# Optimization experiments

Measured on AMD Instinct MI355X. Metric: run time of the kernel, lower is better.

## Reference

```python
import jax, jax.numpy as jnp
import numpy as np

B, N, R, S, H, D, HIDDEN = 4, 1028, 4, 32, 12, 64, 32
L = (2 * S - 1) ** 2  # 3969 relative-position bins


def _build_tables():
    # CPB relative-coordinate table (signed log1p-normalized offsets)
    rng = np.arange(-(S - 1), S, dtype=np.float32)
    dY, dX = np.meshgrid(rng, rng, indexing='ij')
    rel = np.stack([dY / max(S - 1, 1), dX / max(S - 1, 1)], -1).reshape(-1, 2)
    rel_table = np.sign(rel) * np.log1p(np.abs(rel))  # [L, 2]
    # 2D relative-position index table over the SxS patch grid
    Y, X = np.meshgrid(np.arange(S), np.arange(S), indexing='ij')
    flat = np.stack([Y, X], 0).reshape(2, -1)          # [2, P]
    d = flat[:, :, None] - flat[:, None, :]            # [2, P, P]
    d = np.transpose(d, (1, 2, 0)).copy()              # [P, P, 2]
    d[:, :, 0] += S - 1
    d[:, :, 1] += S - 1
    d[:, :, 0] *= 2 * S - 1
    l_idx = d.sum(-1)                                  # [P, P] in [0, L)
    idx = np.full((N, N), -1, dtype=np.int64)          # -1 sentinel for register tokens
    idx[R:, R:] = l_idx
    return jnp.asarray(rel_table, jnp.float32), jnp.asarray(idx)


def setup_inputs() -> dict:
    key = jax.random.key(0)
    ks = jax.random.split(key, 8)
    rel_table, idx_table = _build_tables()
    return {
        'q': jax.random.normal(ks[0], (B, H, N, D), jnp.float32),
        'k': jax.random.normal(ks[1], (B, H, N, D), jnp.float32),
        'v': jax.random.normal(ks[2], (B, H, N, D), jnp.float32),
        'mu': jax.random.normal(ks[3], (B, 2 * H, N), jnp.float32),
        'rel_table': rel_table,                              # [L, 2] buffer
        'W1': jax.random.normal(ks[4], (HIDDEN, 2), jnp.float32) * 0.5,
        'b1': jax.random.normal(ks[5], (HIDDEN,), jnp.float32) * 0.1,
        'W2': jax.random.normal(ks[6], (H, HIDDEN), jnp.float32) * 0.05,
        'gamma': jax.random.normal(ks[7], (H,), jnp.float32),
        'idx_table': idx_table,                              # [N, N] int64
    }


def reference(q, k, v, mu, rel_table, W1, b1, W2, gamma, idx_table):
    # CPB MLP: Linear(2->hidden) + exact GELU + Linear(hidden->H, no bias)
    hid = jax.nn.gelu(rel_table @ W1.T + b1, approximate=False)   # [L, HIDDEN]
    bt = hid @ W2.T                                               # [L, H]
    bt_ext = jnp.concatenate([jnp.zeros((1, H), bt.dtype), bt], 0)  # [L+1, H]
    bias = bt_ext[idx_table + 1]                                  # [N, N, H]; sentinel -1 -> zero row

    # per-token gates: signed log1p transform then q-side + k-side split
    mu_t = jnp.sign(mu) * jnp.log1p(jnp.abs(mu))                  # [B, 2H, N]
    mu_q, mu_k = mu_t[:, :H], mu_t[:, H:]                         # each [B, H, N]
    g = mu_q[:, :, :, None] + mu_k[:, :, None, :]                 # [B, H, N, N]
    gam = jax.nn.sigmoid(gamma)[None, :, None, None]              # [1, H, 1, 1]

    scale = 1.0 / jnp.sqrt(jnp.asarray(D, jnp.float32))
    scores = jnp.einsum('bhqd,bhkd->bhqk', q, k) * scale
    scores = scores + gam * g * jnp.transpose(bias, (2, 0, 1))[None]  # [B, H, N, N]
    attn = jax.nn.softmax(scores, axis=-1)
    return jnp.einsum('bhqk,bhkd->bhqd', attn, v)
```

## Files before the change

kernel.cpp:

```cpp
#include <hip/hip_runtime.h>

#define B_ 4
#define H_ 12
#define N_ 1028
#define D_ 64
#define R_ 4
#define L_ 3969
#define HID_ 32
#define KBLK 64
#define NT_ 17
#define NBH_ (B_*H_)
#define QBLK 256
#define NQT 5
#define NWG (NBH_*NQT)
#define MUTP 1088
#define LOG2E 1.4426950408889634f
#define SCL1 (0.125f*LOG2E)

typedef __attribute__((ext_vector_type(8)))  short bf16x8;
typedef __attribute__((ext_vector_type(2)))  float f32x2;
typedef __attribute__((ext_vector_type(4)))  float f32x4;
typedef __attribute__((ext_vector_type(16))) float f32x16;
typedef __attribute__((ext_vector_type(2)))  unsigned int u32x2;
typedef __attribute__((ext_vector_type(4)))  unsigned int u32x4;

__device__ __forceinline__ unsigned pkbf(float lo, float hi) {
  unsigned r;
  asm("v_cvt_pk_bf16_f32 %0, %1, %2" : "=v"(r) : "v"(lo), "v"(hi));
  return r;
}
__device__ __forceinline__ float exp2_fast(float x) {
  float r; asm("v_exp_f32 %0, %1" : "=v"(r) : "v"(x)); return r;
}
__device__ __forceinline__ float sgnlog1p(float x) {
  float t = log1pf(fabsf(x));
  return (x > 0.f) ? t : ((x < 0.f) ? -t : 0.f);
}

__global__ __launch_bounds__(256) void btmu_kernel(
    const float* __restrict__ rel, const float* __restrict__ W1,
    const float* __restrict__ b1, const float* __restrict__ W2,
    const float* __restrict__ mug, float* __restrict__ bt,
    float* __restrict__ mut) {
  const int blk = blockIdx.x;
  const int tid = threadIdx.x;
  if (blk < 16) {
    int l = blk * 256 + tid;
    if (l >= L_) return;
    float r0 = rel[2*l], r1 = rel[2*l+1];
    float hid[HID_];
#pragma unroll
    for (int j = 0; j < HID_; ++j) {
      float x = W1[2*j]*r0 + W1[2*j+1]*r1 + b1[j];
      hid[j] = 0.5f * x * (1.f + erff(x * 0.70710678118654752f));
    }
#pragma unroll
    for (int h = 0; h < H_; ++h) {
      float acc = 0.f;
#pragma unroll
      for (int j = 0; j < HID_; ++j) acc += W2[h*HID_+j]*hid[j];
      bt[h*L_ + l] = acc;
    }
  } else {
    int idx = (blk - 16) * 256 + tid;
    if (idx >= NBH_*MUTP) return;
    int bh = idx / MUTP, n = idx - bh*MUTP;
    int b = bh / H_, h = bh - b*H_;
    int nc = n < N_ ? n : N_-1;
    mut[bh*MUTP + n] = sgnlog1p(mug[((size_t)b*2*H_ + H_ + h)*N_ + nc]);
  }
}

__global__ __launch_bounds__(512, 2) void attn_kernel(
    const float* __restrict__ qg, const float* __restrict__ kg_,
    const float* __restrict__ vg, const float* __restrict__ mug,
    const float* __restrict__ gammag, const float* __restrict__ btg_g,
    const float* __restrict__ mut, float* __restrict__ outg)
{
  __shared__ __align__(16) float btgs[L_ + 4];
  __shared__ __align__(16) unsigned short Kl[2][64*64];
  __shared__ __align__(16) unsigned short Vl[2][64*64];

  const int tid  = threadIdx.x;
  const int w    = tid >> 6;
  const int lane = tid & 63;
  const int hi   = lane >> 5;
  const int c    = lane & 31;

  const int orig = blockIdx.x;
  const int wg   = (orig & 7) * (NWG/8) + (orig >> 3);
  const int bh   = wg / NQT;
  const int qt   = wg - bh * NQT;
  const int b    = bh / H_;
  const int h    = bh - b * H_;
  const int q0   = qt * QBLK;

  const float gam  = 1.f / (1.f + __expf(-gammag[h]));
  const float gscl = gam * LOG2E;
  for (int i = tid; i < L_; i += 512) btgs[4 + i] = gscl * btg_g[h*L_ + i];
  if (tid < 4) btgs[tid] = 0.f;

  const float* qb = qg  + (size_t)bh*N_*D_;
  const float* kb = kg_ + (size_t)bh*N_*D_;
  const float* vb = vg  + (size_t)bh*N_*D_;
  const float* mt = mut + bh*MUTP;

  const int qrow = q0 + 32*w + c;
  const int qrc  = qrow < N_ ? qrow : N_-1;
  bf16x8 qf[4];
#pragma unroll
  for (int m = 0; m < 4; ++m) {
    const float* p = qb + (size_t)qrc*D_ + 16*m + 8*hi;
    f32x4 a0 = *(const f32x4*)p;
    f32x4 a1 = *(const f32x4*)(p + 4);
    u32x4 qw;
    qw[0] = pkbf(a0[0]*SCL1, a0[1]*SCL1); qw[1] = pkbf(a0[2]*SCL1, a0[3]*SCL1);
    qw[2] = pkbf(a1[0]*SCL1, a1[1]*SCL1); qw[3] = pkbf(a1[2]*SCL1, a1[3]*SCL1);
    qf[m] = __builtin_bit_cast(bf16x8, qw);
  }
  const float muq_c = (qrow < N_) ? sgnlog1p(mug[((size_t)b*2*H_ + h)*N_ + qrow]) : 0.f;
  const int  qi  = qrow - R_;
  const bool qok = (qi >= 0) && (qrow < N_);
  const int  qy  = qi >> 5, qx = qi & 31;
  const int  lqc = qy*63 + qx + 1988;

  const int skr = tid >> 3;
  const int so  = tid & 7;
  const int vkc0 = (tid & 15) * 4;
  const int vdp  = (tid >> 4) * 2;
  const int vkc0p = ((vkc0 >> 1) & 4) | ((vkc0 << 1) & 8) | (vkc0 & 48);

  f32x4 ka0_, ka1_;
  f32x2 vpre[4];
  auto issue = [&](int tt) {
    const int k0n = tt * KBLK;
    {
      int kr = k0n + skr; if (kr >= N_) kr = N_-1;
      const float* p = kb + (size_t)kr*D_ + 8*so;
      ka0_ = *(const f32x4*)p;
      ka1_ = *(const f32x4*)(p + 4);
    }
#pragma unroll
    for (int i = 0; i < 4; ++i) {
      int kr = k0n + vkc0 + i; if (kr >= N_) kr = N_-1;
      vpre[i] = *(const f32x2*)(vb + (size_t)kr*D_ + vdp);
    }
  };

  float mrun = -3.0e38f, lrun = 0.f;
  f32x16 Ot[2];
#pragma unroll
  for (int blk = 0; blk < 2; ++blk)
#pragma unroll
    for (int r = 0; r < 16; ++r) Ot[blk][r] = 0.f;

  issue(0);

  for (int t = 0; t < NT_; ++t) {
    const int k0 = t * KBLK;
    const int p  = t & 1;
    {
      u32x4 kw;
      kw[0] = pkbf(ka0_[0], ka0_[1]); kw[1] = pkbf(ka0_[2], ka0_[3]);
      kw[2] = pkbf(ka1_[0], ka1_[1]); kw[3] = pkbf(ka1_[2], ka1_[3]);
      *(u32x4*)&Kl[p][skr*64 + ((8*so) ^ ((skr & 7) << 3))] = kw;
#pragma unroll
      for (int dd = 0; dd < 2; ++dd) {
        int d = vdp + dd;
        u32x2 vw = (u32x2){pkbf(vpre[0][dd], vpre[1][dd]), pkbf(vpre[2][dd], vpre[3][dd])};
        *(u32x2*)&Vl[p][d*64 + (vkc0p ^ ((d & 7) << 3))] = vw;
      }
    }
    if (t + 1 < NT_) issue(t + 1);
    __syncthreads();

    f32x4 mkv[2][4];
#pragma unroll
    for (int bb = 0; bb < 2; ++bb)
#pragma unroll
      for (int r2 = 0; r2 < 4; ++r2)
        mkv[bb][r2] = *(const f32x4*)&mt[k0 + 32*bb + 8*r2 + 4*hi];

    f32x16 sc[2];
#pragma unroll
    for (int bb = 0; bb < 2; ++bb)
#pragma unroll
      for (int r = 0; r < 16; ++r) sc[bb][r] = 0.f;
    __builtin_amdgcn_s_setprio(1);
#pragma unroll
    for (int m = 0; m < 4; ++m) {
      int sw = (c & 7) << 3;
      bf16x8 ka0 = *(const bf16x8*)&Kl[p][c*64        + ((16*m + 8*hi) ^ sw)];
      bf16x8 ka1 = *(const bf16x8*)&Kl[p][(32+c)*64   + ((16*m + 8*hi) ^ sw)];
      sc[0] = __builtin_amdgcn_mfma_f32_32x32x16_bf16(ka0, qf[m], sc[0], 0, 0, 0);
      sc[1] = __builtin_amdgcn_mfma_f32_32x32x16_bf16(ka1, qf[m], sc[1], 0, 0, 0);
    }
    __builtin_amdgcn_s_setprio(0);

    float smax = -3.0e38f;
#pragma unroll
    for (int bb = 0; bb < 2; ++bb) {
#pragma unroll
      for (int r2 = 0; r2 < 4; ++r2) {
        const f32x4 mk = mkv[bb][r2];
        int base_kc = 32*bb + 8*r2 + 4*hi;
        int ki0 = k0 + base_kc - R_;
        int lk  = (ki0 >> 5)*63 + (ki0 & 31);
        int va  = lqc - lk;
        bool okq = ((unsigned)ki0 < 1024u) && qok;
        int basep = okq ? va : 3;
        f32x4 bv;
        bv[0] = btgs[basep-3]; bv[1] = btgs[basep-2];
        bv[2] = btgs[basep-1]; bv[3] = btgs[basep];
        bool maskq = (ki0 < 1024);
#pragma unroll
        for (int rr = 0; rr < 4; ++rr) {
          float val = sc[bb][4*r2+rr] + (muq_c + mk[rr]) * bv[3-rr];
          val = maskq ? val : -3.0e38f;
          sc[bb][4*r2+rr] = val;
          smax = fmaxf(smax, val);
        }
      }
    }
    smax = fmaxf(smax, __shfl_xor(smax, 32));

    if (__any(smax > mrun)) {
      float mnew = fmaxf(mrun, smax);
      float corr = exp2_fast(mrun - mnew);
      lrun *= corr;
#pragma unroll
      for (int blk = 0; blk < 2; ++blk)
#pragma unroll
        for (int r = 0; r < 16; ++r) Ot[blk][r] *= corr;
      mrun = mnew;
    }

    float psum = 0.f;
#pragma unroll
    for (int bb = 0; bb < 2; ++bb)
#pragma unroll
      for (int r = 0; r < 16; ++r) {
        float pv = exp2_fast(sc[bb][r] - mrun);
        sc[bb][r] = pv;
        psum += pv;
      }
    psum += __shfl_xor(psum, 32);
    lrun += psum;

    u32x4 pa[4];
#pragma unroll
    for (int mm = 0; mm < 4; ++mm) {
      int bb = mm >> 1, s = (mm & 1) * 8;
#pragma unroll
      for (int j = 0; j < 4; ++j)
        pa[mm][j] = pkbf(sc[bb][s + 2*j], sc[bb][s + 2*j + 1]);
    }

    __builtin_amdgcn_s_setprio(1);
#pragma unroll
    for (int mm = 0; mm < 4; ++mm) {
      bf16x8 pfr = __builtin_bit_cast(bf16x8, pa[mm]);
      int sw = (c & 7) << 3;
      bf16x8 va0 = *(const bf16x8*)&Vl[p][c*64      + ((16*mm + 8*hi) ^ sw)];
      bf16x8 va1 = *(const bf16x8*)&Vl[p][(32+c)*64 + ((16*mm + 8*hi) ^ sw)];
      Ot[0] = __builtin_amdgcn_mfma_f32_32x32x16_bf16(va0, pfr, Ot[0], 0, 0, 0);
      Ot[1] = __builtin_amdgcn_mfma_f32_32x32x16_bf16(va1, pfr, Ot[1], 0, 0, 0);
    }
    __builtin_amdgcn_s_setprio(0);
  }

  float rlv = 1.f / lrun;
  const int qo = q0 + 32*w + c;
  if (qo < N_) {
    float* ob = outg + ((size_t)bh*N_ + qo)*D_;
#pragma unroll
    for (int blk = 0; blk < 2; ++blk)
#pragma unroll
      for (int r2 = 0; r2 < 4; ++r2) {
        int dbase = 8*r2 + 4*hi + 32*blk;
        f32x4 ov;
#pragma unroll
        for (int rr = 0; rr < 4; ++rr) ov[rr] = Ot[blk][4*r2+rr] * rlv;
        *(f32x4*)(ob + dbase) = ov;
      }
  }
}

extern "C" void kernel_launch(void* const* d_in, const int* in_sizes, int n_in,
                              void* d_out, int out_size, void* d_ws, size_t ws_size,
                              hipStream_t stream) {
  const float* q     = (const float*)d_in[0];
  const float* k     = (const float*)d_in[1];
  const float* v     = (const float*)d_in[2];
  const float* mu    = (const float*)d_in[3];
  const float* rel   = (const float*)d_in[4];
  const float* W1    = (const float*)d_in[5];
  const float* b1    = (const float*)d_in[6];
  const float* W2    = (const float*)d_in[7];
  const float* gamma = (const float*)d_in[8];

  float* bt  = (float*)d_ws;
  float* mut = bt + H_*L_;

  const int mutblocks = (NBH_*MUTP + 255) / 256;
  btmu_kernel<<<dim3(16 + mutblocks), dim3(256), 0, stream>>>(rel, W1, b1, W2, mu, bt, mut);
  attn_kernel<<<dim3(NWG), dim3(512), 0, stream>>>(q, k, v, mu, gamma, bt, mut,
                                                   (float*)d_out);
}
```

Measured before the change: 61.63 us.

## Split key range across two workgroups with a separate log-sum-exp combine kernel

Each (batch, head, query-tile) attention pass is now split across two workgroups that cover the two halves of the key blocks. Each workgroup writes unnormalized partial outputs plus its running max and sum, and a new combine kernel merges them. Query tiles shrink to 128 rows with 256-thread workgroups, which raises the workgroup count for better CU occupancy. The bias table is stored as bf16 and the gamma scale is folded into the precomputed mu table. The trade-off is an extra kernel launch, partial-output traffic through global memory, and some bf16 rounding of the bias values.

```diff
diff --git a/kernel.cpp b/kernel.cpp
--- a/kernel.cpp
+++ b/kernel.cpp
@@ -9,10 +9,12 @@
 #define HID_ 32
 #define KBLK 64
 #define NT_ 17
-#define NBH_ (B_*H_)
-#define QBLK 256
-#define NQT 5
-#define NWG (NBH_*NQT)
+#define NBH_ 48
+#define QBLK 128
+#define NQT 9
+#define KS_ 2
+#define NWG (NBH_*NQT*KS_)
+#define NROW (NBH_*N_)
 #define MUTP 1088
 #define LOG2E 1.4426950408889634f
 #define SCL1 (0.125f*LOG2E)
@@ -29,6 +31,9 @@
   asm("v_cvt_pk_bf16_f32 %0, %1, %2" : "=v"(r) : "v"(lo), "v"(hi));
   return r;
 }
+__device__ __forceinline__ float b2f(unsigned short u) {
+  return __builtin_bit_cast(float, (unsigned)u << 16);
+}
 __device__ __forceinline__ float exp2_fast(float x) {
   float r; asm("v_exp_f32 %0, %1" : "=v"(r) : "v"(x)); return r;
 }
@@ -40,8 +45,8 @@
 __global__ __launch_bounds__(256) void btmu_kernel(
     const float* __restrict__ rel, const float* __restrict__ W1,
     const float* __restrict__ b1, const float* __restrict__ W2,
-    const float* __restrict__ mug, float* __restrict__ bt,
-    float* __restrict__ mut) {
+    const float* __restrict__ gammag, const float* __restrict__ mug,
+    unsigned short* __restrict__ btw, float* __restrict__ mut) {
   const int blk = blockIdx.x;
   const int tid = threadIdx.x;
   if (blk < 16) {
@@ -59,7 +64,7 @@
       float acc = 0.f;
 #pragma unroll
       for (int j = 0; j < HID_; ++j) acc += W2[h*HID_+j]*hid[j];
-      bt[h*L_ + l] = acc;
+      btw[h*L_ + l] = (unsigned short)(pkbf(acc, acc) & 0xffffu);
     }
   } else {
     int idx = (blk - 16) * 256 + tid;
@@ -67,15 +72,17 @@
     int bh = idx / MUTP, n = idx - bh*MUTP;
     int b = bh / H_, h = bh - b*H_;
     int nc = n < N_ ? n : N_-1;
-    mut[bh*MUTP + n] = sgnlog1p(mug[((size_t)b*2*H_ + H_ + h)*N_ + nc]);
+    float gscl = LOG2E / (1.f + __expf(-gammag[h]));
+    mut[idx] = sgnlog1p(mug[((size_t)b*2*H_ + H_ + h)*N_ + nc]) * gscl;
   }
 }
 
-__global__ __launch_bounds__(512, 2) void attn_kernel(
+__global__ __launch_bounds__(256, 3) void attn_kernel(
     const float* __restrict__ qg, const float* __restrict__ kg_,
     const float* __restrict__ vg, const float* __restrict__ mug,
-    const float* __restrict__ gammag, const float* __restrict__ btg_g,
-    const float* __restrict__ mut, float* __restrict__ outg)
+    const float* __restrict__ gammag, const unsigned short* __restrict__ btw,
+    const float* __restrict__ mut, float* __restrict__ pO1,
+    float* __restrict__ ml0, float* __restrict__ ml1, float* __restrict__ outg)
 {
   __shared__ __align__(16) float btgs[L_ + 4];
   __shared__ __align__(16) unsigned short Kl[2][64*64];
@@ -89,15 +96,18 @@
 
   const int orig = blockIdx.x;
   const int wg   = (orig & 7) * (NWG/8) + (orig >> 3);
-  const int bh   = wg / NQT;
-  const int qt   = wg - bh * NQT;
+  const int bh   = wg / (NQT*KS_);
+  const int rem  = wg - bh*(NQT*KS_);
+  const int qt   = rem >> 1;
+  const int ks   = rem & 1;
   const int b    = bh / H_;
   const int h    = bh - b * H_;
   const int q0   = qt * QBLK;
-
-  const float gam  = 1.f / (1.f + __expf(-gammag[h]));
-  const float gscl = gam * LOG2E;
-  for (int i = tid; i < L_; i += 512) btgs[4 + i] = gscl * btg_g[h*L_ + i];
+  const int tbeg = ks ? 9 : 0;
+  const int tend = ks ? 17 : 9;
+
+  const float gscl = LOG2E / (1.f + __expf(-gammag[h]));
+  for (int i = tid; i < L_; i += 256) btgs[4 + i] = gscl * b2f(btw[h*L_ + i]);
   if (tid < 4) btgs[tid] = 0.f;
 
   const float* qb = qg  + (size_t)bh*N_*D_;
@@ -118,32 +128,31 @@
     qw[2] = pkbf(a1[0]*SCL1, a1[1]*SCL1); qw[3] = pkbf(a1[2]*SCL1, a1[3]*SCL1);
     qf[m] = __builtin_bit_cast(bf16x8, qw);
   }
-  const float muq_c = (qrow < N_) ? sgnlog1p(mug[((size_t)b*2*H_ + h)*N_ + qrow]) : 0.f;
+  const float muq_c = (qrow < N_) ? sgnlog1p(mug[((size_t)b*2*H_ + h)*N_ + qrow]) * gscl : 0.f;
   const int  qi  = qrow - R_;
   const bool qok = (qi >= 0) && (qrow < N_);
   const int  qy  = qi >> 5, qx = qi & 31;
   const int  lqc = qy*63 + qx + 1988;
 
-  const int skr = tid >> 3;
-  const int so  = tid & 7;
+  const int skr  = tid >> 2;
+  const int sgp  = (tid & 3) * 2;
   const int vkc0 = (tid & 15) * 4;
-  const int vdp  = (tid >> 4) * 2;
+  const int vd0  = (tid >> 4) * 4;
   const int vkc0p = ((vkc0 >> 1) & 4) | ((vkc0 << 1) & 8) | (vkc0 & 48);
 
-  f32x4 ka0_, ka1_;
-  f32x2 vpre[4];
+  f32x4 kpre[4], vpre[4];
   auto issue = [&](int tt) {
     const int k0n = tt * KBLK;
     {
       int kr = k0n + skr; if (kr >= N_) kr = N_-1;
-      const float* p = kb + (size_t)kr*D_ + 8*so;
-      ka0_ = *(const f32x4*)p;
-      ka1_ = *(const f32x4*)(p + 4);
+      const float* p = kb + (size_t)kr*D_ + sgp*8;
+      kpre[0] = *(const f32x4*)p;       kpre[1] = *(const f32x4*)(p + 4);
+      kpre[2] = *(const f32x4*)(p + 8); kpre[3] = *(const f32x4*)(p + 12);
     }
 #pragma unroll
     for (int i = 0; i < 4; ++i) {
       int kr = k0n + vkc0 + i; if (kr >= N_) kr = N_-1;
-      vpre[i] = *(const f32x2*)(vb + (size_t)kr*D_ + vdp);
+      vpre[i] = *(const f32x4*)(vb + (size_t)kr*D_ + vd0);
     }
   };
 
@@ -154,24 +163,28 @@
 #pragma unroll
     for (int r = 0; r < 16; ++r) Ot[blk][r] = 0.f;
 
-  issue(0);
-
-  for (int t = 0; t < NT_; ++t) {
+  issue(tbeg);
+
+  for (int t = tbeg; t < tend; ++t) {
     const int k0 = t * KBLK;
-    const int p  = t & 1;
+    const int p  = (t - tbeg) & 1;
     {
-      u32x4 kw;
-      kw[0] = pkbf(ka0_[0], ka0_[1]); kw[1] = pkbf(ka0_[2], ka0_[3]);
-      kw[2] = pkbf(ka1_[0], ka1_[1]); kw[3] = pkbf(ka1_[2], ka1_[3]);
-      *(u32x4*)&Kl[p][skr*64 + ((8*so) ^ ((skr & 7) << 3))] = kw;
-#pragma unroll
-      for (int dd = 0; dd < 2; ++dd) {
-        int d = vdp + dd;
-        u32x2 vw = (u32x2){pkbf(vpre[0][dd], vpre[1][dd]), pkbf(vpre[2][dd], vpre[3][dd])};
+      const int sw = (skr & 7) << 3;
+      u32x4 kw0, kw1;
+      kw0[0] = pkbf(kpre[0][0], kpre[0][1]); kw0[1] = pkbf(kpre[0][2], kpre[0][3]);
+      kw0[2] = pkbf(kpre[1][0], kpre[1][1]); kw0[3] = pkbf(kpre[1][2], kpre[1][3]);
+      kw1[0] = pkbf(kpre[2][0], kpre[2][1]); kw1[1] = pkbf(kpre[2][2], kpre[2][3]);
+      kw1[2] = pkbf(kpre[3][0], kpre[3][1]); kw1[3] = pkbf(kpre[3][2], kpre[3][3]);
+      *(u32x4*)&Kl[p][skr*64 + ((sgp*8) ^ sw)]       = kw0;
+      *(u32x4*)&Kl[p][skr*64 + (((sgp+1)*8) ^ sw)]   = kw1;
+#pragma unroll
+      for (int j = 0; j < 4; ++j) {
+        int d = vd0 + j;
+        u32x2 vw = (u32x2){pkbf(vpre[0][j], vpre[1][j]), pkbf(vpre[2][j], vpre[3][j])};
         *(u32x2*)&Vl[p][d*64 + (vkc0p ^ ((d & 7) << 3))] = vw;
       }
     }
-    if (t + 1 < NT_) issue(t + 1);
+    if (t + 1 < tend) issue(t + 1);
     __syncthreads();
 
     f32x4 mkv[2][4];
@@ -190,8 +203,8 @@
 #pragma unroll
     for (int m = 0; m < 4; ++m) {
       int sw = (c & 7) << 3;
-      bf16x8 ka0 = *(const bf16x8*)&Kl[p][c*64        + ((16*m + 8*hi) ^ sw)];
-      bf16x8 ka1 = *(const bf16x8*)&Kl[p][(32+c)*64   + ((16*m + 8*hi) ^ sw)];
+      bf16x8 ka0 = *(const bf16x8*)&Kl[p][c*64      + ((16*m + 8*hi) ^ sw)];
+      bf16x8 ka1 = *(const bf16x8*)&Kl[p][(32+c)*64 + ((16*m + 8*hi) ^ sw)];
       sc[0] = __builtin_amdgcn_mfma_f32_32x32x16_bf16(ka0, qf[m], sc[0], 0, 0, 0);
       sc[1] = __builtin_amdgcn_mfma_f32_32x32x16_bf16(ka1, qf[m], sc[1], 0, 0, 0);
     }
@@ -269,10 +282,10 @@
     __builtin_amdgcn_s_setprio(0);
   }
 
-  float rlv = 1.f / lrun;
   const int qo = q0 + 32*w + c;
   if (qo < N_) {
-    float* ob = outg + ((size_t)bh*N_ + qo)*D_;
+    const int row = bh*N_ + qo;
+    float* ob = (ks == 0 ? outg : pO1) + (size_t)row*64;
 #pragma unroll
     for (int blk = 0; blk < 2; ++blk)
 #pragma unroll
@@ -280,10 +293,33 @@
         int dbase = 8*r2 + 4*hi + 32*blk;
         f32x4 ov;
 #pragma unroll
-        for (int rr = 0; rr < 4; ++rr) ov[rr] = Ot[blk][4*r2+rr] * rlv;
+        for (int rr = 0; rr < 4; ++rr) ov[rr] = Ot[blk][4*r2+rr];
         *(f32x4*)(ob + dbase) = ov;
       }
+    if (hi == 0) {
+      float* mlp_ = (ks == 0 ? ml0 : ml1) + (size_t)row*2;
+      mlp_[0] = mrun; mlp_[1] = lrun;
+    }
   }
+}
+
+__global__ __launch_bounds__(256) void comb_kernel(
+    const float* __restrict__ pO1, const float* __restrict__ ml0,
+    const float* __restrict__ ml1, float* __restrict__ outg) {
+  int idx = blockIdx.x*256 + threadIdx.x;
+  int row = idx >> 4;
+  int d4  = (idx & 15) * 4;
+  float m0 = ml0[(size_t)row*2], l0 = ml0[(size_t)row*2+1];
+  float m1 = ml1[(size_t)row*2], l1 = ml1[(size_t)row*2+1];
+  float M  = fmaxf(m0, m1);
+  float w0 = exp2_fast(m0 - M), w1 = exp2_fast(m1 - M);
+  float rl = 1.f / (l0*w0 + l1*w1);
+  f32x4 o0 = *(const f32x4*)(outg + (size_t)row*64 + d4);
+  f32x4 o1 = *(const f32x4*)(pO1  + (size_t)row*64 + d4);
+  f32x4 of;
+#pragma unroll
+  for (int j = 0; j < 4; ++j) of[j] = (o0[j]*w0 + o1[j]*w1) * rl;
+  *(f32x4*)(outg + (size_t)row*64 + d4) = of;
 }
 
 extern "C" void kernel_launch(void* const* d_in, const int* in_sizes, int n_in,
@@ -299,11 +335,16 @@
   const float* W2    = (const float*)d_in[7];
   const float* gamma = (const float*)d_in[8];
 
-  float* bt  = (float*)d_ws;
-  float* mut = bt + H_*L_;
+  char* wsb = (char*)d_ws;
+  unsigned short* btw = (unsigned short*)wsb;
+  float* mut = (float*)(wsb + 95264);
+  float* ml0 = (float*)(wsb + 304160);
+  float* ml1 = (float*)(wsb + 698912);
+  float* pO1 = (float*)(wsb + 1093664);
 
   const int mutblocks = (NBH_*MUTP + 255) / 256;
-  btmu_kernel<<<dim3(16 + mutblocks), dim3(256), 0, stream>>>(rel, W1, b1, W2, mu, bt, mut);
-  attn_kernel<<<dim3(NWG), dim3(512), 0, stream>>>(q, k, v, mu, gamma, bt, mut,
-                                                   (float*)d_out);
-}
+  btmu_kernel<<<dim3(16 + mutblocks), dim3(256), 0, stream>>>(rel, W1, b1, W2, gamma, mu, btw, mut);
+  attn_kernel<<<dim3(NWG), dim3(256), 0, stream>>>(q, k, v, mu, gamma, btw, mut,
+                                                   pO1, ml0, ml1, (float*)d_out);
+  comb_kernel<<<dim3(NROW*16/256), dim3(256), 0, stream>>>(pO1, ml0, ml1, (float*)d_out);
+}
```

New measurement: 114.7 us. +86.1%, slower.
